# Kernel tuning notes

Measured on AMD Instinct MI355X. Metric: run time of the kernel, lower is better.

Reference implementation:

```python
import jax, jax.numpy as jnp
import numpy as np

B, S, H, I, SI, E, TOPK = 2, 1024, 1024, 512, 2048, 8, 2


def setup_inputs() -> dict:
    key = jax.random.key(0)
    ks = jax.random.split(key, 8)
    w = 0.02
    return {
        "hidden_states": jax.random.normal(ks[0], (B, S, H), jnp.float32),
        "router_weight": jax.random.normal(ks[1], (E, H), jnp.float32) * w,
        "gate_up_proj": jax.random.normal(ks[2], (E, 2 * I, H), jnp.float32) * w,
        "down_proj": jax.random.normal(ks[3], (E, H, I), jnp.float32) * w,
        "shared_gate_w": jax.random.normal(ks[4], (SI, H), jnp.float32) * w,
        "shared_up_w": jax.random.normal(ks[5], (SI, H), jnp.float32) * w,
        "shared_down_w": jax.random.normal(ks[6], (H, SI), jnp.float32) * w,
        "shared_expert_gate_w": jax.random.normal(ks[7], (1, H), jnp.float32) * w,
    }


def reference(hidden_states, router_weight, gate_up_proj, down_proj,
              shared_gate_w, shared_up_w, shared_down_w, shared_expert_gate_w):
    b, s, h = hidden_states.shape
    x = hidden_states.reshape(-1, h)  # [T, H]

    # shared expert (SwiGLU)
    shared = (jax.nn.silu(x @ shared_gate_w.T) * (x @ shared_up_w.T)) @ shared_down_w.T  # [T, H]

    # top-k softmax router (softmax in fp32, renormalized top-k weights)
    logits = x @ router_weight.T  # [T, E]
    probs = jax.nn.softmax(logits.astype(jnp.float32), axis=-1)
    top_v, top_i = jax.lax.top_k(probs, TOPK)
    top_v = (top_v / jnp.sum(top_v, axis=-1, keepdims=True)).astype(logits.dtype)  # [T, K]

    # combine weights per (token, expert): sum over k of routing weight * one_hot
    cw = jnp.sum(jax.nn.one_hot(top_i, E, dtype=top_v.dtype) * top_v[..., None], axis=1)  # [T, E]

    # grouped-expert SwiGLU (dense compute, masked combine == gather/scatter math)
    gu = jnp.einsum('th,eih->eti', x, gate_up_proj)  # [E, T, 2I]
    gate, up = jnp.split(gu, 2, axis=-1)
    act = jax.nn.silu(gate) * up  # [E, T, I]
    per_expert = jnp.einsum('eti,ehi->eth', act, down_proj)  # [E, T, H]
    expert_out = jnp.einsum('eth,te->th', per_expert, cw)  # [T, H]

    out = expert_out + jax.nn.sigmoid(x @ shared_expert_gate_w.T) * shared
    return out.reshape(b, s, h)
```

## Files before the change

kernel.cpp:

```cpp
#include <hip/hip_runtime.h>

#define T_TOK 2048
#define H_DIM 1024
#define I_DIM 512
#define SI_DIM 2048
#define E_NUM 8
#define NSLOT 4096

typedef __attribute__((ext_vector_type(8))) short short8;
typedef __attribute__((ext_vector_type(4))) float floatx4;

__device__ inline unsigned short f2bf(float f) {
  unsigned u = __builtin_bit_cast(unsigned, f);
  u = (u + 0x7FFFu + ((u >> 16) & 1u)) >> 16;
  return (unsigned short)u;
}
__device__ inline float bf2f(unsigned short u) {
  return __builtin_bit_cast(float, (unsigned)u << 16);
}

__device__ inline void gl_lds16(const void* g, void* l) {
  __builtin_amdgcn_global_load_lds(
      (const __attribute__((address_space(1))) unsigned int*)g,
      (__attribute__((address_space(3))) unsigned int*)l, 16, 0, 0);
}

__global__ __launch_bounds__(256) void cast_router(
    const float* __restrict__ x, const float* __restrict__ rw,
    const float* __restrict__ segw,
    const float* __restrict__ s1, const float* __restrict__ s2,
    const float* __restrict__ s3, const float* __restrict__ s4,
    const float* __restrict__ s5,
    unsigned short* __restrict__ d0, unsigned short* __restrict__ d1,
    unsigned short* __restrict__ d2, unsigned short* __restrict__ d3,
    unsigned short* __restrict__ d4, unsigned short* __restrict__ d5,
    int* __restrict__ top2, float2* __restrict__ w01, float* __restrict__ sg) {
  const int bid = blockIdx.x;
  if (bid < 512) {
    int t = bid * 4 + (threadIdx.x >> 6);
    int lane = threadIdx.x & 63;
    const float* xt = x + (long)t * H_DIM;
    float xv[16];
#pragma unroll
    for (int j = 0; j < 16; ++j) xv[j] = xt[j * 64 + lane];
    float dots[9];
#pragma unroll
    for (int e = 0; e < 8; ++e) {
      const float* w = rw + e * H_DIM;
      float s = 0.f;
#pragma unroll
      for (int j = 0; j < 16; ++j) s += xv[j] * w[j * 64 + lane];
      dots[e] = s;
    }
    {
      float s = 0.f;
#pragma unroll
      for (int j = 0; j < 16; ++j) s += xv[j] * segw[j * 64 + lane];
      dots[8] = s;
    }
#pragma unroll
    for (int off = 32; off > 0; off >>= 1) {
#pragma unroll
      for (int e = 0; e < 9; ++e) dots[e] += __shfl_xor(dots[e], off, 64);
    }
    if (lane == 0) {
      int e0 = 0;
      for (int e = 1; e < 8; ++e)
        if (dots[e] > dots[e0]) e0 = e;
      int e1 = (e0 == 0) ? 1 : 0;
      for (int e = 0; e < 8; ++e)
        if (e != e0 && dots[e] > dots[e1]) e1 = e;
      float p1 = expf(dots[e1] - dots[e0]);
      top2[t] = e0 | (e1 << 8);
      w01[t] = make_float2(1.f / (1.f + p1), p1 / (1.f + p1));
      sg[t] = 1.f / (1.f + expf(-dots[8]));
    }
  } else {
    long g = (long)(bid - 512) * 256 + threadIdx.x;
    const float* s;
    unsigned short* d;
    long off;
    if (g < 524288L)       { s = x;  d = d0; off = g; }
    else if (g < 2621440L) { s = s1; d = d1; off = g - 524288L; }
    else if (g < 3670016L) { s = s2; d = d2; off = g - 2621440L; }
    else if (g < 4194304L) { s = s3; d = d3; off = g - 3670016L; }
    else if (g < 4718592L) { s = s4; d = d4; off = g - 4194304L; }
    else                   { s = s5; d = d5; off = g - 4718592L; }
    float4 v = ((const float4*)s)[off];
    ushort4 o;
    o.x = f2bf(v.x); o.y = f2bf(v.y); o.z = f2bf(v.z); o.w = f2bf(v.w);
    ((ushort4*)d)[off] = o;
  }
}

__global__ __launch_bounds__(256) void build_lists(
    const int* __restrict__ top2, int* __restrict__ cnt, int* __restrict__ ebase,
    int* __restrict__ slot_token, int* __restrict__ tok_slot) {
  const int e = blockIdx.x;
  const int tid = threadIdx.x;
  const int lane = tid & 63, wid = tid >> 6;
  __shared__ int wsum[4], wbelow[4];
  const int base_t = tid * 8;
  int mk[8], kk[8];
  int c = 0, below = 0;
#pragma unroll
  for (int j = 0; j < 8; ++j) {
    int p = top2[base_t + j];
    int e0 = p & 0xFF, e1 = (p >> 8) & 0xFF;
    below += (e0 < e) + (e1 < e);
    int m = 0, k = 0;
    if (e0 == e) { m = 1; k = 0; }
    else if (e1 == e) { m = 1; k = 1; }
    mk[j] = m; kk[j] = k;
    c += m;
  }
  int inc = c;
#pragma unroll
  for (int off = 1; off < 64; off <<= 1) {
    int n = __shfl_up(inc, off, 64);
    if (lane >= off) inc += n;
  }
  int bsum = below;
#pragma unroll
  for (int off = 32; off > 0; off >>= 1) bsum += __shfl_xor(bsum, off, 64);
  if (lane == 63) wsum[wid] = inc;
  if (lane == 0) wbelow[wid] = bsum;
  __syncthreads();
  int woff = 0;
#pragma unroll
  for (int i = 0; i < 4; ++i)
    if (i < wid) woff += wsum[i];
  int baseE = wbelow[0] + wbelow[1] + wbelow[2] + wbelow[3];
  int pos = baseE + woff + inc - c;
#pragma unroll
  for (int j = 0; j < 8; ++j) {
    if (mk[j]) {
      slot_token[pos] = base_t + j;
      tok_slot[2 * (base_t + j) + kk[j]] = pos;
      pos++;
    }
  }
  if (tid == 255) cnt[e] = woff + inc;
  if (tid == 0) ebase[e] = baseE;
}

template <bool GATHER>
__device__ __forceinline__ void swiglu_body(
    char* smem, int bx, int by, int e,
    const unsigned short* __restrict__ A, const unsigned short* __restrict__ Bg,
    const unsigned short* __restrict__ Bu, unsigned short* __restrict__ Out,
    const int* __restrict__ slot_token, const int* __restrict__ cnt,
    const int* __restrict__ ebase, int N, int K, long estrideB) {
  const int BM = 128, BK = 32;
  const int tid = threadIdx.x;
  const int lane = tid & 63;
  const int wid = tid >> 6;
  const int wm = wid & 1;
  const int wn = wid >> 1;
  const int m0 = by * BM;
  const int n0 = bx * 64;
  int Meff = 0, baseE = 0;
  if (GATHER) {
    Meff = cnt[e];
    if (m0 >= Meff) return;
    baseE = ebase[e];
  }
  const unsigned short* BgE = Bg + (long)e * estrideB;
  const unsigned short* BuE = Bu + (long)e * estrideB;

  unsigned short* As = (unsigned short*)smem;
  unsigned short* Bgs = As + 2 * BM * BK;
  unsigned short* Bus = Bgs + 2 * 64 * BK;

  const int lrow = lane >> 2;
  const int lcol = (((lane & 3) ^ ((lrow >> 1) & 3)) << 4);

  const char* aP[2];
#pragma unroll
  for (int i = 0; i < 2; ++i) {
    int m = m0 + wid * 32 + i * 16 + lrow;
    long row;
    if (GATHER) {
      int mm = (m < Meff - 1) ? m : (Meff - 1);
      row = slot_token[baseE + mm];
    } else {
      row = m;
    }
    aP[i] = (const char*)A + row * (long)(K * 2) + lcol;
  }
  int nb = n0 + wid * 16 + lrow;
  const char* bgP = (const char*)BgE + (long)nb * (K * 2) + lcol;
  const char* buP = (const char*)BuE + (long)nb * (K * 2) + lcol;

  floatx4 accG[4][2], accU[4][2];
  floatx4 zero = {0.f, 0.f, 0.f, 0.f};
#pragma unroll
  for (int i = 0; i < 4; ++i)
#pragma unroll
    for (int j = 0; j < 2; ++j) { accG[i][j] = zero; accU[i][j] = zero; }

  const int ar = lane & 15;
  const int aksw = (((lane >> 4) ^ ((ar >> 1) & 3)) << 3);

  auto stage = [&](int p, int k0) {
#pragma unroll
    for (int i = 0; i < 2; ++i)
      gl_lds16(aP[i] + (long)k0 * 2, &As[p * BM * BK + (wid * 32 + i * 16) * BK]);
    gl_lds16(bgP + (long)k0 * 2, &Bgs[p * 64 * BK + (wid * 16) * BK]);
    gl_lds16(buP + (long)k0 * 2, &Bus[p * 64 * BK + (wid * 16) * BK]);
  };

  stage(0, 0);
  const int NI = K / BK;
  for (int i = 0; i < NI; ++i) {
    __syncthreads();
    if (i + 1 < NI) stage((i + 1) & 1, (i + 1) * BK);
    const unsigned short* Ab = &As[(i & 1) * BM * BK];
    const unsigned short* Gb = &Bgs[(i & 1) * 64 * BK];
    const unsigned short* Ub = &Bus[(i & 1) * 64 * BK];
    short8 af[4], bgf[2], buf2[2];
#pragma unroll
    for (int tm = 0; tm < 4; ++tm)
      af[tm] = *(const short8*)&Ab[(wm * 64 + tm * 16 + ar) * BK + aksw];
#pragma unroll
    for (int tn = 0; tn < 2; ++tn) {
      bgf[tn] = *(const short8*)&Gb[(wn * 32 + tn * 16 + ar) * BK + aksw];
      buf2[tn] = *(const short8*)&Ub[(wn * 32 + tn * 16 + ar) * BK + aksw];
    }
#pragma unroll
    for (int tm = 0; tm < 4; ++tm)
#pragma unroll
      for (int tn = 0; tn < 2; ++tn) {
        accG[tm][tn] = __builtin_amdgcn_mfma_f32_16x16x32_bf16(af[tm], bgf[tn], accG[tm][tn], 0, 0, 0);
        accU[tm][tn] = __builtin_amdgcn_mfma_f32_16x16x32_bf16(af[tm], buf2[tn], accU[tm][tn], 0, 0, 0);
      }
  }

#pragma unroll
  for (int tm = 0; tm < 4; ++tm)
#pragma unroll
    for (int tn = 0; tn < 2; ++tn)
#pragma unroll
      for (int r = 0; r < 4; ++r) {
        int row = m0 + wm * 64 + tm * 16 + (lane >> 4) * 4 + r;
        int col = n0 + wn * 32 + tn * 16 + (lane & 15);
        if (!GATHER || row < Meff) {
          float g = accG[tm][tn][r];
          float u = accU[tm][tn][r];
          float act = g / (1.f + expf(-g)) * u;
          Out[(long)(baseE + row) * N + col] = f2bf(act);
        }
      }
}

__global__ __launch_bounds__(256, 2) void swiglu_fused(
    const unsigned short* __restrict__ xb, const unsigned short* __restrict__ sgate,
    const unsigned short* __restrict__ sup, unsigned short* __restrict__ act_s,
    const unsigned short* __restrict__ gup, unsigned short* __restrict__ act_e,
    const int* __restrict__ slot_token, const int* __restrict__ cnt,
    const int* __restrict__ ebase) {
  __shared__ __align__(16) char smem[32768];
  int bid = blockIdx.x;
  if (bid < 512) {
    swiglu_body<false>(smem, bid & 31, bid >> 5, 0, xb, sgate, sup, act_s,
                       nullptr, nullptr, nullptr, SI_DIM, H_DIM, 0);
  } else {
    int b2 = bid - 512;
    int e = b2 >> 7;
    int rem = b2 & 127;
    swiglu_body<true>(smem, rem & 7, rem >> 3, e, xb, gup,
                      gup + (long)I_DIM * H_DIM, act_e, slot_token, cnt,
                      ebase, I_DIM, H_DIM, (long)2 * I_DIM * H_DIM);
  }
}

template <int MODE>
__device__ __forceinline__ void down_body(
    char* smem, int bx, int by, int e,
    const unsigned short* __restrict__ A, const unsigned short* __restrict__ B,
    float* __restrict__ OutF, unsigned short* __restrict__ OutB,
    const int* __restrict__ ebase, const int* __restrict__ cnt,
    int N, int Kstride, int kbeg, int kcnt, long estrideB) {
  const int BM = 128, BK = 32;
  const int tid = threadIdx.x;
  const int lane = tid & 63;
  const int wid = tid >> 6;
  const int wm = wid & 1;
  const int wn = wid >> 1;
  const int m0 = by * BM;
  const int n0 = bx * 128;
  int Meff = 0, baseE = 0;
  if (MODE == 1) {
    Meff = cnt[e];
    if (m0 >= Meff) return;
    baseE = ebase[e];
  }
  const unsigned short* BE = B + (long)e * estrideB;

  unsigned short* As = (unsigned short*)smem;
  unsigned short* Bs = As + 2 * BM * BK;

  const int lrow = lane >> 2;
  const int lcol = (((lane & 3) ^ ((lrow >> 1) & 3)) << 4);

  const char* aP[2];
  const char* bP[2];
#pragma unroll
  for (int i = 0; i < 2; ++i) {
    int m = m0 + wid * 32 + i * 16 + lrow;
    long arow;
    if (MODE == 1) {
      int mm = (m < Meff - 1) ? m : (Meff - 1);
      arow = baseE + mm;
    } else {
      arow = m;
    }
    aP[i] = (const char*)A + arow * (long)(Kstride * 2) + (long)kbeg * 2 + lcol;
    int n = n0 + wid * 32 + i * 16 + lrow;
    bP[i] = (const char*)BE + (long)n * (Kstride * 2) + (long)kbeg * 2 + lcol;
  }

  floatx4 acc[4][4];
  floatx4 zero = {0.f, 0.f, 0.f, 0.f};
#pragma unroll
  for (int i = 0; i < 4; ++i)
#pragma unroll
    for (int j = 0; j < 4; ++j) acc[i][j] = zero;

  const int ar = lane & 15;
  const int aksw = (((lane >> 4) ^ ((ar >> 1) & 3)) << 3);

  auto stage = [&](int p, int k0) {
#pragma unroll
    for (int i = 0; i < 2; ++i) {
      gl_lds16(aP[i] + (long)k0 * 2, &As[p * BM * BK + (wid * 32 + i * 16) * BK]);
      gl_lds16(bP[i] + (long)k0 * 2, &Bs[p * BM * BK + (wid * 32 + i * 16) * BK]);
    }
  };

  stage(0, 0);
  const int NI = kcnt / BK;
  for (int i = 0; i < NI; ++i) {
    __syncthreads();
    if (i + 1 < NI) stage((i + 1) & 1, (i + 1) * BK);
    const unsigned short* Ab = &As[(i & 1) * BM * BK];
    const unsigned short* Bb = &Bs[(i & 1) * BM * BK];
    short8 af[4], bf[4];
#pragma unroll
    for (int tm = 0; tm < 4; ++tm)
      af[tm] = *(const short8*)&Ab[(wm * 64 + tm * 16 + ar) * BK + aksw];
#pragma unroll
    for (int tn = 0; tn < 4; ++tn)
      bf[tn] = *(const short8*)&Bb[(wn * 64 + tn * 16 + ar) * BK + aksw];
#pragma unroll
    for (int tm = 0; tm < 4; ++tm)
#pragma unroll
      for (int tn = 0; tn < 4; ++tn)
        acc[tm][tn] = __builtin_amdgcn_mfma_f32_16x16x32_bf16(af[tm], bf[tn], acc[tm][tn], 0, 0, 0);
  }

#pragma unroll
  for (int tm = 0; tm < 4; ++tm)
#pragma unroll
    for (int r = 0; r < 4; ++r) {
      int row = m0 + wm * 64 + tm * 16 + (lane >> 4) * 4 + r;
#pragma unroll
      for (int tn = 0; tn < 4; ++tn) {
        int col = n0 + wn * 64 + tn * 16 + (lane & 15);
        float v = acc[tm][tn][r];
        if (MODE == 0) {
          OutF[(long)row * N + col] = v;
        } else if (MODE == 2) {
          OutB[(long)row * N + col] = f2bf(v);
        } else if (row < Meff) {
          OutB[(long)(baseE + row) * N + col] = f2bf(v);
        }
      }
    }
}

__global__ __launch_bounds__(256, 2) void down_fused(
    const unsigned short* __restrict__ act_s, const unsigned short* __restrict__ sdown,
    float* __restrict__ out, unsigned short* __restrict__ spart,
    const unsigned short* __restrict__ act_e, const unsigned short* __restrict__ downw,
    unsigned short* __restrict__ eout, const int* __restrict__ ebase,
    const int* __restrict__ cnt) {
  __shared__ __align__(16) char smem[32768];
  int bid = blockIdx.x;
  if (bid < 128) {
    down_body<0>(smem, bid & 7, bid >> 3, 0, act_s, sdown, out, nullptr,
                 nullptr, nullptr, H_DIM, SI_DIM, 0, 1024, 0);
  } else if (bid < 256) {
    int b = bid - 128;
    down_body<2>(smem, b & 7, b >> 3, 0, act_s, sdown, nullptr, spart,
                 nullptr, nullptr, H_DIM, SI_DIM, 1024, 1024, 0);
  } else {
    int b2 = bid - 256;
    int e = b2 >> 7;
    int rem = b2 & 127;
    down_body<1>(smem, rem & 7, rem >> 3, e, act_e, downw, nullptr, eout,
                 ebase, cnt, H_DIM, I_DIM, 0, I_DIM, (long)H_DIM * I_DIM);
  }
}

__global__ __launch_bounds__(256) void combine_kernel(
    float* __restrict__ out, const unsigned short* __restrict__ spart,
    const unsigned short* __restrict__ eout, const float* __restrict__ sg,
    const float2* __restrict__ w01, const int* __restrict__ tok_slot) {
  int t = blockIdx.x;
  int c = threadIdx.x;
  float sgr = sg[t];
  float2 wr = w01[t];
  int s0 = tok_slot[2 * t];
  int s1 = tok_slot[2 * t + 1];
  ushort4 p1 = ((const ushort4*)(spart + (long)t * H_DIM))[c];
  ushort4 e0 = ((const ushort4*)(eout + (long)s0 * H_DIM))[c];
  ushort4 e1 = ((const ushort4*)(eout + (long)s1 * H_DIM))[c];
  float4* op = &((float4*)(out + (long)t * H_DIM))[c];
  float4 o = *op;
  o.x = sgr * (o.x + bf2f(p1.x)) + wr.x * bf2f(e0.x) + wr.y * bf2f(e1.x);
  o.y = sgr * (o.y + bf2f(p1.y)) + wr.x * bf2f(e0.y) + wr.y * bf2f(e1.y);
  o.z = sgr * (o.z + bf2f(p1.z)) + wr.x * bf2f(e0.z) + wr.y * bf2f(e1.z);
  o.w = sgr * (o.w + bf2f(p1.w)) + wr.x * bf2f(e0.w) + wr.y * bf2f(e1.w);
  *op = o;
}

extern "C" void kernel_launch(void* const* d_in, const int* in_sizes, int n_in,
                              void* d_out, int out_size, void* d_ws, size_t ws_size,
                              hipStream_t stream) {
  const float* x = (const float*)d_in[0];
  const float* rw = (const float*)d_in[1];
  const float* gup = (const float*)d_in[2];
  const float* dwn = (const float*)d_in[3];
  const float* sgw = (const float*)d_in[4];
  const float* suw = (const float*)d_in[5];
  const float* sdw = (const float*)d_in[6];
  const float* segw = (const float*)d_in[7];
  float* out = (float*)d_out;

  char* w = (char*)d_ws;
  unsigned short* xb = (unsigned short*)(w + 0);
  unsigned short* gup_b = (unsigned short*)(w + 4194304L);
  unsigned short* down_b = (unsigned short*)(w + 20971520L);
  unsigned short* sgate_b = (unsigned short*)(w + 29360128L);
  unsigned short* sup_b = (unsigned short*)(w + 33554432L);
  unsigned short* sdown_b = (unsigned short*)(w + 37748736L);
  unsigned short* act_s = (unsigned short*)(w + 41943040L);
  unsigned short* act_e = (unsigned short*)(w + 50331648L);
  unsigned short* eout = (unsigned short*)(w + 54525952L);
  float* sg = (float*)(w + 62914560L);
  int* top2 = (int*)(w + 62922752L);
  float2* w01 = (float2*)(w + 62930944L);
  int* cnt = (int*)(w + 62947328L);
  int* ebase = (int*)(w + 62947584L);
  int* slot_token = (int*)(w + 62947840L);
  int* tok_slot = (int*)(w + 62964224L);
  unsigned short* spart = xb;

  cast_router<<<20992, 256, 0, stream>>>(x, rw, segw, gup, dwn, sgw, suw, sdw,
                                         xb, gup_b, down_b, sgate_b, sup_b,
                                         sdown_b, top2, w01, sg);
  build_lists<<<E_NUM, 256, 0, stream>>>(top2, cnt, ebase, slot_token, tok_slot);
  swiglu_fused<<<1536, 256, 0, stream>>>(xb, sgate_b, sup_b, act_s, gup_b,
                                         act_e, slot_token, cnt, ebase);
  down_fused<<<1280, 256, 0, stream>>>(act_s, sdown_b, out, spart, act_e,
                                       down_b, eout, ebase, cnt);
  combine_kernel<<<T_TOK, 256, 0, stream>>>(out, spart, eout, sg, w01, tok_slot);
}
```

Before: 208.4 us.

## Double GEMM block tiles to 256xBN with 512-thread blocks in swiglu and down kernels

Both the fused SwiGLU and down-projection GEMM kernels move to 512-thread blocks (8 waves) with a 256-row M tile. The shared SwiGLU uses a 128-column N tile, and the expert SwiGLU uses a 64-column tile where half the waves load gate and half load up. Larger tiles raise reuse of each staged A/B tile and cut the number of blocks and redundant global loads. In exchange, LDS use per block doubles (64KB / 48KB), which may lower occupancy, and fewer blocks for small expert groups may waste more work on padded rows.

```diff
diff --git a/kernel.cpp b/kernel.cpp
--- a/kernel.cpp
+++ b/kernel.cpp
@@ -144,21 +144,24 @@
   if (tid == 0) ebase[e] = baseE;
 }
 
-template <bool GATHER>
+template <bool GATHER, int BN>
 __device__ __forceinline__ void swiglu_body(
     char* smem, int bx, int by, int e,
     const unsigned short* __restrict__ A, const unsigned short* __restrict__ Bg,
     const unsigned short* __restrict__ Bu, unsigned short* __restrict__ Out,
     const int* __restrict__ slot_token, const int* __restrict__ cnt,
     const int* __restrict__ ebase, int N, int K, long estrideB) {
-  const int BM = 128, BK = 32;
+  constexpr int BM = 256, BK = 32;
+  constexpr int NT = BN / 32;
+  constexpr int ATILE = BM * BK;
+  constexpr int BTILE = BN * BK;
   const int tid = threadIdx.x;
   const int lane = tid & 63;
   const int wid = tid >> 6;
-  const int wm = wid & 1;
-  const int wn = wid >> 1;
+  const int wm = wid & 3;
+  const int wn = wid >> 2;
   const int m0 = by * BM;
-  const int n0 = bx * 64;
+  const int n0 = bx * BN;
   int Meff = 0, baseE = 0;
   if (GATHER) {
     Meff = cnt[e];
@@ -169,8 +172,8 @@
   const unsigned short* BuE = Bu + (long)e * estrideB;
 
   unsigned short* As = (unsigned short*)smem;
-  unsigned short* Bgs = As + 2 * BM * BK;
-  unsigned short* Bus = Bgs + 2 * 64 * BK;
+  unsigned short* Bgs = As + 2 * ATILE;
+  unsigned short* Bus = Bgs + 2 * BTILE;
 
   const int lrow = lane >> 2;
   const int lcol = (((lane & 3) ^ ((lrow >> 1) & 3)) << 4);
@@ -188,16 +191,28 @@
     }
     aP[i] = (const char*)A + row * (long)(K * 2) + lcol;
   }
-  int nb = n0 + wid * 16 + lrow;
-  const char* bgP = (const char*)BgE + (long)nb * (K * 2) + lcol;
-  const char* buP = (const char*)BuE + (long)nb * (K * 2) + lcol;
-
-  floatx4 accG[4][2], accU[4][2];
+  const char* bgP = nullptr;
+  const char* buP = nullptr;
+  const char* bsP = nullptr;
+  unsigned short* bDst = nullptr;
+  if constexpr (BN == 128) {
+    int n = n0 + wid * 16 + lrow;
+    bgP = (const char*)BgE + (long)n * (K * 2) + lcol;
+    buP = (const char*)BuE + (long)n * (K * 2) + lcol;
+  } else {
+    int cw = wid & 3;
+    int n = n0 + cw * 16 + lrow;
+    const unsigned short* src = (wid < 4) ? BgE : BuE;
+    bsP = (const char*)src + (long)n * (K * 2) + lcol;
+    bDst = ((wid < 4) ? Bgs : Bus) + cw * 16 * BK;
+  }
+
+  floatx4 accG[4][NT], accU[4][NT];
   floatx4 zero = {0.f, 0.f, 0.f, 0.f};
 #pragma unroll
   for (int i = 0; i < 4; ++i)
 #pragma unroll
-    for (int j = 0; j < 2; ++j) { accG[i][j] = zero; accU[i][j] = zero; }
+    for (int j = 0; j < NT; ++j) { accG[i][j] = zero; accU[i][j] = zero; }
 
   const int ar = lane & 15;
   const int aksw = (((lane >> 4) ^ ((ar >> 1) & 3)) << 3);
@@ -205,9 +220,13 @@
   auto stage = [&](int p, int k0) {
 #pragma unroll
     for (int i = 0; i < 2; ++i)
-      gl_lds16(aP[i] + (long)k0 * 2, &As[p * BM * BK + (wid * 32 + i * 16) * BK]);
-    gl_lds16(bgP + (long)k0 * 2, &Bgs[p * 64 * BK + (wid * 16) * BK]);
-    gl_lds16(buP + (long)k0 * 2, &Bus[p * 64 * BK + (wid * 16) * BK]);
+      gl_lds16(aP[i] + (long)k0 * 2, &As[p * ATILE + (wid * 32 + i * 16) * BK]);
+    if constexpr (BN == 128) {
+      gl_lds16(bgP + (long)k0 * 2, &Bgs[p * BTILE + (wid * 16) * BK]);
+      gl_lds16(buP + (long)k0 * 2, &Bus[p * BTILE + (wid * 16) * BK]);
+    } else {
+      gl_lds16(bsP + (long)k0 * 2, bDst + p * BTILE);
+    }
   };
 
   stage(0, 0);
@@ -215,22 +234,22 @@
   for (int i = 0; i < NI; ++i) {
     __syncthreads();
     if (i + 1 < NI) stage((i + 1) & 1, (i + 1) * BK);
-    const unsigned short* Ab = &As[(i & 1) * BM * BK];
-    const unsigned short* Gb = &Bgs[(i & 1) * 64 * BK];
-    const unsigned short* Ub = &Bus[(i & 1) * 64 * BK];
-    short8 af[4], bgf[2], buf2[2];
+    const unsigned short* Ab = &As[(i & 1) * ATILE];
+    const unsigned short* Gb = &Bgs[(i & 1) * BTILE];
+    const unsigned short* Ub = &Bus[(i & 1) * BTILE];
+    short8 af[4], bgf[NT], buf2[NT];
 #pragma unroll
     for (int tm = 0; tm < 4; ++tm)
       af[tm] = *(const short8*)&Ab[(wm * 64 + tm * 16 + ar) * BK + aksw];
 #pragma unroll
-    for (int tn = 0; tn < 2; ++tn) {
-      bgf[tn] = *(const short8*)&Gb[(wn * 32 + tn * 16 + ar) * BK + aksw];
-      buf2[tn] = *(const short8*)&Ub[(wn * 32 + tn * 16 + ar) * BK + aksw];
+    for (int tn = 0; tn < NT; ++tn) {
+      bgf[tn] = *(const short8*)&Gb[(wn * (BN / 2) + tn * 16 + ar) * BK + aksw];
+      buf2[tn] = *(const short8*)&Ub[(wn * (BN / 2) + tn * 16 + ar) * BK + aksw];
     }
 #pragma unroll
     for (int tm = 0; tm < 4; ++tm)
 #pragma unroll
-      for (int tn = 0; tn < 2; ++tn) {
+      for (int tn = 0; tn < NT; ++tn) {
         accG[tm][tn] = __builtin_amdgcn_mfma_f32_16x16x32_bf16(af[tm], bgf[tn], accG[tm][tn], 0, 0, 0);
         accU[tm][tn] = __builtin_amdgcn_mfma_f32_16x16x32_bf16(af[tm], buf2[tn], accU[tm][tn], 0, 0, 0);
       }
@@ -239,11 +258,11 @@
 #pragma unroll
   for (int tm = 0; tm < 4; ++tm)
 #pragma unroll
-    for (int tn = 0; tn < 2; ++tn)
+    for (int tn = 0; tn < NT; ++tn)
 #pragma unroll
       for (int r = 0; r < 4; ++r) {
         int row = m0 + wm * 64 + tm * 16 + (lane >> 4) * 4 + r;
-        int col = n0 + wn * 32 + tn * 16 + (lane & 15);
+        int col = n0 + wn * (BN / 2) + tn * 16 + (lane & 15);
         if (!GATHER || row < Meff) {
           float g = accG[tm][tn][r];
           float u = accU[tm][tn][r];
@@ -253,24 +272,24 @@
       }
 }
 
-__global__ __launch_bounds__(256, 2) void swiglu_fused(
+__global__ __launch_bounds__(512, 2) void swiglu_fused(
     const unsigned short* __restrict__ xb, const unsigned short* __restrict__ sgate,
     const unsigned short* __restrict__ sup, unsigned short* __restrict__ act_s,
     const unsigned short* __restrict__ gup, unsigned short* __restrict__ act_e,
     const int* __restrict__ slot_token, const int* __restrict__ cnt,
     const int* __restrict__ ebase) {
-  __shared__ __align__(16) char smem[32768];
+  __shared__ __align__(16) char smem[65536];
   int bid = blockIdx.x;
-  if (bid < 512) {
-    swiglu_body<false>(smem, bid & 31, bid >> 5, 0, xb, sgate, sup, act_s,
-                       nullptr, nullptr, nullptr, SI_DIM, H_DIM, 0);
+  if (bid < 128) {
+    swiglu_body<false, 128>(smem, bid & 15, bid >> 4, 0, xb, sgate, sup, act_s,
+                            nullptr, nullptr, nullptr, SI_DIM, H_DIM, 0);
   } else {
-    int b2 = bid - 512;
-    int e = b2 >> 7;
-    int rem = b2 & 127;
-    swiglu_body<true>(smem, rem & 7, rem >> 3, e, xb, gup,
-                      gup + (long)I_DIM * H_DIM, act_e, slot_token, cnt,
-                      ebase, I_DIM, H_DIM, (long)2 * I_DIM * H_DIM);
+    int b2 = bid - 128;
+    int e = b2 >> 6;
+    int rem = b2 & 63;
+    swiglu_body<true, 64>(smem, rem & 7, rem >> 3, e, xb, gup,
+                          gup + (long)I_DIM * H_DIM, act_e, slot_token, cnt,
+                          ebase, I_DIM, H_DIM, (long)2 * I_DIM * H_DIM);
   }
 }
 
@@ -281,14 +300,16 @@
     float* __restrict__ OutF, unsigned short* __restrict__ OutB,
     const int* __restrict__ ebase, const int* __restrict__ cnt,
     int N, int Kstride, int kbeg, int kcnt, long estrideB) {
-  const int BM = 128, BK = 32;
+  constexpr int BM = 256, BN = 128, BK = 32;
+  constexpr int ATILE = BM * BK;
+  constexpr int BTILE = BN * BK;
   const int tid = threadIdx.x;
   const int lane = tid & 63;
   const int wid = tid >> 6;
-  const int wm = wid & 1;
-  const int wn = wid >> 1;
+  const int wm = wid & 3;
+  const int wn = wid >> 2;
   const int m0 = by * BM;
-  const int n0 = bx * 128;
+  const int n0 = bx * BN;
   int Meff = 0, baseE = 0;
   if (MODE == 1) {
     Meff = cnt[e];
@@ -298,13 +319,12 @@
   const unsigned short* BE = B + (long)e * estrideB;
 
   unsigned short* As = (unsigned short*)smem;
-  unsigned short* Bs = As + 2 * BM * BK;
+  unsigned short* Bs = As + 2 * ATILE;
 
   const int lrow = lane >> 2;
   const int lcol = (((lane & 3) ^ ((lrow >> 1) & 3)) << 4);
 
   const char* aP[2];
-  const char* bP[2];
 #pragma unroll
   for (int i = 0; i < 2; ++i) {
     int m = m0 + wid * 32 + i * 16 + lrow;
@@ -316,9 +336,9 @@
       arow = m;
     }
     aP[i] = (const char*)A + arow * (long)(Kstride * 2) + (long)kbeg * 2 + lcol;
-    int n = n0 + wid * 32 + i * 16 + lrow;
-    bP[i] = (const char*)BE + (long)n * (Kstride * 2) + (long)kbeg * 2 + lcol;
-  }
+  }
+  int nb = n0 + wid * 16 + lrow;
+  const char* bP = (const char*)BE + (long)nb * (Kstride * 2) + (long)kbeg * 2 + lcol;
 
   floatx4 acc[4][4];
   floatx4 zero = {0.f, 0.f, 0.f, 0.f};
@@ -332,10 +352,9 @@
 
   auto stage = [&](int p, int k0) {
 #pragma unroll
-    for (int i = 0; i < 2; ++i) {
-      gl_lds16(aP[i] + (long)k0 * 2, &As[p * BM * BK + (wid * 32 + i * 16) * BK]);
-      gl_lds16(bP[i] + (long)k0 * 2, &Bs[p * BM * BK + (wid * 32 + i * 16) * BK]);
-    }
+    for (int i = 0; i < 2; ++i)
+      gl_lds16(aP[i] + (long)k0 * 2, &As[p * ATILE + (wid * 32 + i * 16) * BK]);
+    gl_lds16(bP + (long)k0 * 2, &Bs[p * BTILE + (wid * 16) * BK]);
   };
 
   stage(0, 0);
@@ -343,8 +362,8 @@
   for (int i = 0; i < NI; ++i) {
     __syncthreads();
     if (i + 1 < NI) stage((i + 1) & 1, (i + 1) * BK);
-    const unsigned short* Ab = &As[(i & 1) * BM * BK];
-    const unsigned short* Bb = &Bs[(i & 1) * BM * BK];
+    const unsigned short* Ab = &As[(i & 1) * ATILE];
+    const unsigned short* Bb = &Bs[(i & 1) * BTILE];
     short8 af[4], bf[4];
 #pragma unroll
     for (int tm = 0; tm < 4; ++tm)
@@ -379,25 +398,27 @@
     }
 }
 
-__global__ __launch_bounds__(256, 2) void down_fused(
+__global__ __launch_bounds__(512, 2) void down_fused(
     const unsigned short* __restrict__ act_s, const unsigned short* __restrict__ sdown,
     float* __restrict__ out, unsigned short* __restrict__ spart,
     const unsigned short* __restrict__ act_e, const unsigned short* __restrict__ downw,
     unsigned short* __restrict__ eout, const int* __restrict__ ebase,
     const int* __restrict__ cnt) {
-  __shared__ __align__(16) char smem[32768];
+  __shared__ __align__(16) char smem[49152];
   int bid = blockIdx.x;
   if (bid < 128) {
-    down_body<0>(smem, bid & 7, bid >> 3, 0, act_s, sdown, out, nullptr,
-                 nullptr, nullptr, H_DIM, SI_DIM, 0, 1024, 0);
-  } else if (bid < 256) {
-    int b = bid - 128;
-    down_body<2>(smem, b & 7, b >> 3, 0, act_s, sdown, nullptr, spart,
-                 nullptr, nullptr, H_DIM, SI_DIM, 1024, 1024, 0);
+    int ks = bid >> 6;
+    int rem = bid & 63;
+    if (ks == 0)
+      down_body<0>(smem, rem & 7, rem >> 3, 0, act_s, sdown, out, nullptr,
+                   nullptr, nullptr, H_DIM, SI_DIM, 0, 1024, 0);
+    else
+      down_body<2>(smem, rem & 7, rem >> 3, 0, act_s, sdown, nullptr, spart,
+                   nullptr, nullptr, H_DIM, SI_DIM, 1024, 1024, 0);
   } else {
-    int b2 = bid - 256;
-    int e = b2 >> 7;
-    int rem = b2 & 127;
+    int b2 = bid - 128;
+    int e = b2 >> 6;
+    int rem = b2 & 63;
     down_body<1>(smem, rem & 7, rem >> 3, e, act_e, downw, nullptr, eout,
                  ebase, cnt, H_DIM, I_DIM, 0, I_DIM, (long)H_DIM * I_DIM);
   }
@@ -461,9 +482,9 @@
                                          xb, gup_b, down_b, sgate_b, sup_b,
                                          sdown_b, top2, w01, sg);
   build_lists<<<E_NUM, 256, 0, stream>>>(top2, cnt, ebase, slot_token, tok_slot);
-  swiglu_fused<<<1536, 256, 0, stream>>>(xb, sgate_b, sup_b, act_s, gup_b,
-                                         act_e, slot_token, cnt, ebase);
-  down_fused<<<1280, 256, 0, stream>>>(act_s, sdown_b, out, spart, act_e,
-                                       down_b, eout, ebase, cnt);
+  swiglu_fused<<<640, 512, 0, stream>>>(xb, sgate_b, sup_b, act_s, gup_b,
+                                        act_e, slot_token, cnt, ebase);
+  down_fused<<<640, 512, 0, stream>>>(act_s, sdown_b, out, spart, act_e,
+                                      down_b, eout, ebase, cnt);
   combine_kernel<<<T_TOK, 256, 0, stream>>>(out, spart, eout, sg, w01, tok_slot);
 }
```

After: 211.4 us. No clear change (+1.5%).
